# Kernel tuning notes

Measured on AMD Instinct MI355X. Metric: run time of the kernel, lower is better.

Reference implementation:

```python
import jax, jax.numpy as jnp
import numpy as np

TEMPERATURE = 1.0  # init kwarg
B, D = 8192, 128


def setup_inputs() -> dict:
    key = jax.random.key(0)
    k1, k2 = jax.random.split(key)
    sk = jax.random.normal(k1, (B, D), dtype=jnp.float32)
    im = jax.random.normal(k2, (B, D), dtype=jnp.float32)
    return {"sk": sk, "im": im}


def reference(sk, im):
    # The torch module builds a [2B,2B] Euclidean distance matrix over the
    # interleaved [sk_0, im_0, sk_1, im_1, ...] rows, then via the eye-mask /
    # repeat_interleave / [:,1::2] / good_indices / [::2] gather chain selects,
    # for each anchor i, logits row = [-d(sk_i, im_i)/T] ++ [-d(sk_i, im_j)/T, j != i]
    # with label 0, followed by mean cross-entropy.  Since cross-entropy only
    # depends on {row values} and which entry is positive, this is exactly:
    #   loss = mean_i( logsumexp_j(-d(sk_i, im_j)/T) - (-d(sk_i, im_i)/T) )
    # so we only need the [B,B] sk-vs-im distance block (dist_type == 0).
    sq = (
        jnp.sum(sk * sk, axis=1)[:, None]
        + jnp.sum(im * im, axis=1)[None, :]
        - 2.0 * (sk @ im.T)
    )  # [B, B] squared distances
    d = jnp.sqrt(jnp.maximum(sq, 0.0))
    logits = -d / TEMPERATURE  # [B, B]
    lse = jax.nn.logsumexp(logits, axis=1)  # [B]
    loss = jnp.mean(lse - jnp.diagonal(logits))
    return loss
```

## Files before the change

### kernel.cpp

```cpp
#include <hip/hip_runtime.h>
#include <math.h>

#define NB 8192
#define ND 128
#define NJB 64

typedef __bf16 bf16x8 __attribute__((ext_vector_type(8)));
typedef float f32x4 __attribute__((ext_vector_type(4)));

typedef __attribute__((address_space(3))) void lds_void_t;
typedef __attribute__((address_space(1))) const void gconst_void_t;

__device__ __forceinline__ unsigned f2bf(float f) {
    union { float f; unsigned u; } v; v.f = f;
    unsigned r = v.u + 0x7FFFu + ((v.u >> 16) & 1u);
    return r >> 16;
}

__global__ void __launch_bounds__(256) prep_kernel(
    const float* __restrict__ sk, const float* __restrict__ im,
    unsigned* __restrict__ skb, unsigned* __restrict__ imb,
    float* __restrict__ skn, float* __restrict__ imn,
    float* __restrict__ diag, float* __restrict__ gacc,
    unsigned* __restrict__ ticket) {
    if (blockIdx.x == 0 && threadIdx.x == 0) { *gacc = 0.f; *ticket = 0u; }
    const int row = blockIdx.x * 4 + (threadIdx.x >> 6);
    const int l = threadIdx.x & 63;
    const size_t off = (size_t)row * ND + l * 2;
    const float2 a = *reinterpret_cast<const float2*>(sk + off);
    const float2 b = *reinterpret_cast<const float2*>(im + off);
    skb[row * 64 + l] = f2bf(a.x) | (f2bf(a.y) << 16);
    imb[row * 64 + l] = f2bf(b.x) | (f2bf(b.y) << 16);
    float sa = a.x * a.x + a.y * a.y;
    float sb = b.x * b.x + b.y * b.y;
    float dx = a.x - b.x, dy = a.y - b.y;
    float sd = dx * dx + dy * dy;
#pragma unroll
    for (int st = 1; st < 64; st <<= 1) {
        sa += __shfl_xor(sa, st);
        sb += __shfl_xor(sb, st);
        sd += __shfl_xor(sd, st);
    }
    if (l == 0) { skn[row] = sa; imn[row] = sb; diag[row] = sqrtf(sd); }
}

__global__ void __launch_bounds__(256) tile_kernel(
    const unsigned short* __restrict__ skb, const unsigned short* __restrict__ imb,
    const float* __restrict__ skn, const float* __restrict__ imn,
    float* __restrict__ partial) {
    __shared__ unsigned short Alds[128 * 128];
    __shared__ unsigned short Blds[128 * 128];
    __shared__ float lds_part[2][128];

    const int t = threadIdx.x;
    const int w = t >> 6, lane = t & 63;
    const int tI = blockIdx.x * 128;
    const int tJ = blockIdx.y * 128;

    {
        const unsigned short* gsrc = (w < 2) ? imb : skb;
        const int half = w & 1;
        const int grow0 = ((w < 2) ? tJ : tI) + half * 64;
        unsigned short* ldst = ((w < 2) ? Alds : Blds) + half * 64 * ND;
#pragma unroll
        for (int q = 0; q < 16; ++q) {
            const int rl = q * 4 + (lane >> 4);
            const int cs = (lane & 15) ^ (rl & 7);
            const unsigned short* gp = gsrc + (size_t)(grow0 + rl) * ND + cs * 8;
            __builtin_amdgcn_global_load_lds((gconst_void_t*)gp,
                                             (lds_void_t*)(ldst + q * 4 * ND),
                                             16, 0, 0);
        }
    }

    const int wr = w >> 1, wc = w & 1;
    const int hi = lane >> 4, lo = lane & 15;
    const int ibase = tI + wc * 64;
    const int jbase = tJ + wr * 64;

    float skv[4];
#pragma unroll
    for (int n = 0; n < 4; ++n) skv[n] = skn[ibase + n * 16 + lo];
    float imnv[4][4];
#pragma unroll
    for (int m = 0; m < 4; ++m) {
        float4 v = *reinterpret_cast<const float4*>(imn + jbase + m * 16 + hi * 4);
        imnv[m][0] = v.x; imnv[m][1] = v.y; imnv[m][2] = v.z; imnv[m][3] = v.w;
    }

    __syncthreads();

    f32x4 acc[4][4];
#pragma unroll
    for (int m = 0; m < 4; ++m)
#pragma unroll
        for (int n = 0; n < 4; ++n)
            acc[m][n] = (f32x4){0.f, 0.f, 0.f, 0.f};

    const char* Ab = (const char*)Alds;
    const char* Bb = (const char*)Blds;
    const int swz = (lo & 7) << 4;
#pragma unroll
    for (int kk = 0; kk < 4; ++kk) {
        const int kb = (kk * 64 + hi * 16) ^ swz;
        bf16x8 af[4], bfr[4];
#pragma unroll
        for (int m = 0; m < 4; ++m)
            af[m] = *reinterpret_cast<const bf16x8*>(Ab + (wr * 64 + m * 16 + lo) * 256 + kb);
#pragma unroll
        for (int n = 0; n < 4; ++n)
            bfr[n] = *reinterpret_cast<const bf16x8*>(Bb + (wc * 64 + n * 16 + lo) * 256 + kb);
#pragma unroll
        for (int m = 0; m < 4; ++m)
#pragma unroll
            for (int n = 0; n < 4; ++n)
                acc[m][n] = __builtin_amdgcn_mfma_f32_16x16x32_bf16(af[m], bfr[n], acc[m][n], 0, 0, 0);
    }

#pragma unroll
    for (int n = 0; n < 4; ++n) {
        float s = 0.f;
#pragma unroll
        for (int m = 0; m < 4; ++m) {
#pragma unroll
            for (int r = 0; r < 4; ++r) {
                float sq = fmaf(-2.f, acc[m][n][r], skv[n] + imnv[m][r]);
                sq = fmaxf(sq, 0.f);
                float d;
                asm("v_sqrt_f32 %0, %1" : "=v"(d) : "v"(sq));
                float x = -1.442695041f * d;
                float e;
                asm("v_exp_f32 %0, %1" : "=v"(e) : "v"(x));
                s += e;
            }
        }
        s += __shfl_xor(s, 16);
        s += __shfl_xor(s, 32);
        if (lane < 16) lds_part[wr][wc * 64 + n * 16 + lane] = s;
    }
    __syncthreads();
    if (t < 128)
        partial[(size_t)(tI + t) * NJB + blockIdx.y] =
            lds_part[0][t] + lds_part[1][t];
}

__global__ void finalize_kernel(const float* __restrict__ partial,
                                const float* __restrict__ diag,
                                float* __restrict__ gacc, unsigned* __restrict__ ticket,
                                float* __restrict__ out) {
    const int i = blockIdx.x * 256 + threadIdx.x;
    const float4* p4 = reinterpret_cast<const float4*>(partial + (size_t)i * NJB);
    float rs = 0.f;
#pragma unroll
    for (int q = 0; q < NJB / 4; ++q) {
        float4 v = p4[q];
        rs += (v.x + v.y) + (v.z + v.w);
    }
    float v = __logf(rs) + diag[i];
    __shared__ float red[256];
    red[threadIdx.x] = v;
    __syncthreads();
    for (int st = 128; st > 0; st >>= 1) {
        if (threadIdx.x < st) red[threadIdx.x] += red[threadIdx.x + st];
        __syncthreads();
    }
    if (threadIdx.x == 0) {
        atomicAdd(gacc, red[0]);
        __threadfence();
        unsigned old = atomicAdd(ticket, 1u);
        if (old == (NB / 256) - 1) {
            float tot = atomicAdd(gacc, 0.f);
            out[0] = tot / (float)NB;
        }
    }
}

extern "C" void kernel_launch(void* const* d_in, const int* in_sizes, int n_in,
                              void* d_out, int out_size, void* d_ws, size_t ws_size,
                              hipStream_t stream) {
    const float* sk = (const float*)d_in[0];
    const float* im = (const float*)d_in[1];
    float* out = (float*)d_out;
    float* ws = (float*)d_ws;

    unsigned short* skb = (unsigned short*)ws;
    unsigned short* imb = skb + (size_t)NB * ND;
    float* fbase   = ws + (size_t)NB * ND;
    float* skn     = fbase;
    float* imn     = fbase + NB;
    float* diag    = fbase + 2 * NB;
    float* partial = fbase + 3 * NB;
    float* gacc    = partial + (size_t)NB * NJB;
    unsigned* ticket = (unsigned*)(gacc + 1);

    prep_kernel<<<NB / 4, 256, 0, stream>>>(
        sk, im, (unsigned*)skb, (unsigned*)imb, skn, imn, diag, gacc, ticket);
    dim3 grid(NB / 128, NB / 128);
    tile_kernel<<<grid, 256, 0, stream>>>(skb, imb, skn, imn, partial);
    finalize_kernel<<<NB / 256, 256, 0, stream>>>(partial, diag, gacc, ticket, out);
}
```

Baseline: 101.6 us.

## Use 512-thread tiles, fold log2e into norms, widen prep loads

The tile kernel now runs 8 waves of 512 threads over the same 128x128 tile. Each wave holds a 4x2 set of MFMA accumulators instead of 4x4, which lowers register pressure and adds waves to hide latency. The log2(e) factor is folded into the squared norms and the -2 coefficient, so the epilogue drops a multiply and negates inside v_exp. The LDS swizzle changes to a 16-way XOR, and the prep kernel uses float4 loads with two rows per wave. The trade is that each wave now amortises its LDS fragment reads over fewer MFMAs.

```diff
diff --git a/kernel.cpp b/kernel.cpp
--- a/kernel.cpp
+++ b/kernel.cpp
@@ -4,6 +4,9 @@
 #define NB 8192
 #define ND 128
 #define NJB 64
+
+#define C2F 2.0813689810056077f
+#define NC2 (-4.1627379620112154f)
 
 typedef __bf16 bf16x8 __attribute__((ext_vector_type(8)));
 typedef float f32x4 __attribute__((ext_vector_type(4)));
@@ -19,53 +22,62 @@
 
 __global__ void __launch_bounds__(256) prep_kernel(
     const float* __restrict__ sk, const float* __restrict__ im,
-    unsigned* __restrict__ skb, unsigned* __restrict__ imb,
+    unsigned short* __restrict__ skb, unsigned short* __restrict__ imb,
     float* __restrict__ skn, float* __restrict__ imn,
     float* __restrict__ diag, float* __restrict__ gacc,
     unsigned* __restrict__ ticket) {
     if (blockIdx.x == 0 && threadIdx.x == 0) { *gacc = 0.f; *ticket = 0u; }
-    const int row = blockIdx.x * 4 + (threadIdx.x >> 6);
-    const int l = threadIdx.x & 63;
-    const size_t off = (size_t)row * ND + l * 2;
-    const float2 a = *reinterpret_cast<const float2*>(sk + off);
-    const float2 b = *reinterpret_cast<const float2*>(im + off);
-    skb[row * 64 + l] = f2bf(a.x) | (f2bf(a.y) << 16);
-    imb[row * 64 + l] = f2bf(b.x) | (f2bf(b.y) << 16);
-    float sa = a.x * a.x + a.y * a.y;
-    float sb = b.x * b.x + b.y * b.y;
-    float dx = a.x - b.x, dy = a.y - b.y;
-    float sd = dx * dx + dy * dy;
-#pragma unroll
-    for (int st = 1; st < 64; st <<= 1) {
+    const int wave = threadIdx.x >> 6, lane = threadIdx.x & 63;
+    const int half = lane >> 5, l32 = lane & 31;
+    const int row = blockIdx.x * 8 + wave * 2 + half;
+    const size_t off = (size_t)row * ND + l32 * 4;
+    const float4 a = *reinterpret_cast<const float4*>(sk + off);
+    const float4 b = *reinterpret_cast<const float4*>(im + off);
+    ushort4 pa, pb;
+    pa.x = (unsigned short)f2bf(a.x); pa.y = (unsigned short)f2bf(a.y);
+    pa.z = (unsigned short)f2bf(a.z); pa.w = (unsigned short)f2bf(a.w);
+    pb.x = (unsigned short)f2bf(b.x); pb.y = (unsigned short)f2bf(b.y);
+    pb.z = (unsigned short)f2bf(b.z); pb.w = (unsigned short)f2bf(b.w);
+    *reinterpret_cast<ushort4*>(skb + off) = pa;
+    *reinterpret_cast<ushort4*>(imb + off) = pb;
+    float sa = a.x * a.x + a.y * a.y + a.z * a.z + a.w * a.w;
+    float sb = b.x * b.x + b.y * b.y + b.z * b.z + b.w * b.w;
+    float dx = a.x - b.x, dy = a.y - b.y, dz = a.z - b.z, dw = a.w - b.w;
+    float sd = dx * dx + dy * dy + dz * dz + dw * dw;
+#pragma unroll
+    for (int st = 1; st < 32; st <<= 1) {
         sa += __shfl_xor(sa, st);
         sb += __shfl_xor(sb, st);
         sd += __shfl_xor(sd, st);
     }
-    if (l == 0) { skn[row] = sa; imn[row] = sb; diag[row] = sqrtf(sd); }
-}
-
-__global__ void __launch_bounds__(256) tile_kernel(
+    if (l32 == 0) {
+        skn[row] = sa * C2F;
+        imn[row] = sb * C2F;
+        diag[row] = sqrtf(sd);
+    }
+}
+
+__global__ void __launch_bounds__(512, 4) tile_kernel(
     const unsigned short* __restrict__ skb, const unsigned short* __restrict__ imb,
     const float* __restrict__ skn, const float* __restrict__ imn,
     float* __restrict__ partial) {
-    __shared__ unsigned short Alds[128 * 128];
-    __shared__ unsigned short Blds[128 * 128];
+    __shared__ unsigned short tiles[256 * 128];
     __shared__ float lds_part[2][128];
 
     const int t = threadIdx.x;
     const int w = t >> 6, lane = t & 63;
+    const int hi = lane >> 4, lo = lane & 15;
     const int tI = blockIdx.x * 128;
     const int tJ = blockIdx.y * 128;
 
     {
-        const unsigned short* gsrc = (w < 2) ? imb : skb;
-        const int half = w & 1;
-        const int grow0 = ((w < 2) ? tJ : tI) + half * 64;
-        unsigned short* ldst = ((w < 2) ? Alds : Blds) + half * 64 * ND;
-#pragma unroll
-        for (int q = 0; q < 16; ++q) {
-            const int rl = q * 4 + (lane >> 4);
-            const int cs = (lane & 15) ^ (rl & 7);
+        const unsigned short* gsrc = (w < 4) ? imb : skb;
+        const int grow0 = ((w < 4) ? tJ : tI) + (w & 3) * 32;
+        unsigned short* ldst = tiles + (size_t)w * 32 * ND;
+#pragma unroll
+        for (int q = 0; q < 8; ++q) {
+            const int rl = q * 4 + hi;
+            const int cs = lo ^ (rl & 15);
             const unsigned short* gp = gsrc + (size_t)(grow0 + rl) * ND + cs * 8;
             __builtin_amdgcn_global_load_lds((gconst_void_t*)gp,
                                              (lds_void_t*)(ldst + q * 4 * ND),
@@ -73,70 +85,66 @@
         }
     }
 
-    const int wr = w >> 1, wc = w & 1;
-    const int hi = lane >> 4, lo = lane & 15;
-    const int ibase = tI + wc * 64;
+    const int wr = w >> 2, wc = w & 3;
+    const int ibase = tI + wc * 32;
     const int jbase = tJ + wr * 64;
 
-    float skv[4];
-#pragma unroll
-    for (int n = 0; n < 4; ++n) skv[n] = skn[ibase + n * 16 + lo];
-    float imnv[4][4];
+    float skv2[2];
+#pragma unroll
+    for (int n = 0; n < 2; ++n) skv2[n] = skn[ibase + n * 16 + lo];
+    float imnv2[4][4];
 #pragma unroll
     for (int m = 0; m < 4; ++m) {
         float4 v = *reinterpret_cast<const float4*>(imn + jbase + m * 16 + hi * 4);
-        imnv[m][0] = v.x; imnv[m][1] = v.y; imnv[m][2] = v.z; imnv[m][3] = v.w;
+        imnv2[m][0] = v.x; imnv2[m][1] = v.y; imnv2[m][2] = v.z; imnv2[m][3] = v.w;
     }
 
     __syncthreads();
 
-    f32x4 acc[4][4];
+    f32x4 acc[4][2];
 #pragma unroll
     for (int m = 0; m < 4; ++m)
 #pragma unroll
-        for (int n = 0; n < 4; ++n)
+        for (int n = 0; n < 2; ++n)
             acc[m][n] = (f32x4){0.f, 0.f, 0.f, 0.f};
 
-    const char* Ab = (const char*)Alds;
-    const char* Bb = (const char*)Blds;
-    const int swz = (lo & 7) << 4;
+    const char* Tb = (const char*)tiles;
 #pragma unroll
     for (int kk = 0; kk < 4; ++kk) {
-        const int kb = (kk * 64 + hi * 16) ^ swz;
-        bf16x8 af[4], bfr[4];
+        const int cb = ((kk * 4 + hi) ^ lo) << 4;
+        bf16x8 af[4], bfr[2];
 #pragma unroll
         for (int m = 0; m < 4; ++m)
-            af[m] = *reinterpret_cast<const bf16x8*>(Ab + (wr * 64 + m * 16 + lo) * 256 + kb);
-#pragma unroll
-        for (int n = 0; n < 4; ++n)
-            bfr[n] = *reinterpret_cast<const bf16x8*>(Bb + (wc * 64 + n * 16 + lo) * 256 + kb);
+            af[m] = *reinterpret_cast<const bf16x8*>(Tb + (wr * 64 + m * 16 + lo) * 256 + cb);
+#pragma unroll
+        for (int n = 0; n < 2; ++n)
+            bfr[n] = *reinterpret_cast<const bf16x8*>(Tb + (128 + wc * 32 + n * 16 + lo) * 256 + cb);
 #pragma unroll
         for (int m = 0; m < 4; ++m)
 #pragma unroll
-            for (int n = 0; n < 4; ++n)
+            for (int n = 0; n < 2; ++n)
                 acc[m][n] = __builtin_amdgcn_mfma_f32_16x16x32_bf16(af[m], bfr[n], acc[m][n], 0, 0, 0);
     }
 
 #pragma unroll
-    for (int n = 0; n < 4; ++n) {
+    for (int n = 0; n < 2; ++n) {
         float s = 0.f;
 #pragma unroll
         for (int m = 0; m < 4; ++m) {
 #pragma unroll
             for (int r = 0; r < 4; ++r) {
-                float sq = fmaf(-2.f, acc[m][n][r], skv[n] + imnv[m][r]);
-                sq = fmaxf(sq, 0.f);
-                float d;
-                asm("v_sqrt_f32 %0, %1" : "=v"(d) : "v"(sq));
-                float x = -1.442695041f * d;
+                float sq2 = fmaf(NC2, acc[m][n][r], skv2[n]) + imnv2[m][r];
+                sq2 = fmaxf(sq2, 0.f);
+                float d2;
+                asm("v_sqrt_f32 %0, %1" : "=v"(d2) : "v"(sq2));
                 float e;
-                asm("v_exp_f32 %0, %1" : "=v"(e) : "v"(x));
+                asm("v_exp_f32 %0, -%1" : "=v"(e) : "v"(d2));
                 s += e;
             }
         }
         s += __shfl_xor(s, 16);
         s += __shfl_xor(s, 32);
-        if (lane < 16) lds_part[wr][wc * 64 + n * 16 + lane] = s;
+        if (lane < 16) lds_part[wr][wc * 32 + n * 16 + lane] = s;
     }
     __syncthreads();
     if (t < 128)
@@ -193,9 +201,9 @@
     float* gacc    = partial + (size_t)NB * NJB;
     unsigned* ticket = (unsigned*)(gacc + 1);
 
-    prep_kernel<<<NB / 4, 256, 0, stream>>>(
-        sk, im, (unsigned*)skb, (unsigned*)imb, skn, imn, diag, gacc, ticket);
+    prep_kernel<<<NB / 8, 256, 0, stream>>>(
+        sk, im, skb, imb, skn, imn, diag, gacc, ticket);
     dim3 grid(NB / 128, NB / 128);
-    tile_kernel<<<grid, 256, 0, stream>>>(skb, imb, skn, imn, partial);
+    tile_kernel<<<grid, 512, 0, stream>>>(skb, imb, skn, imn, partial);
     finalize_kernel<<<NB / 256, 256, 0, stream>>>(partial, diag, gacc, ticket, out);
 }
```

Measured after the change: 98.04 us. 3.5% less time.
